# Performance work log

Measured on AMD Instinct MI355X. Metric: run time of the kernel, lower is better.

The kernel has to match this reference:

```python
import jax, jax.numpy as jnp
import numpy as np
from jax import lax

B, T, H, W, C = 32, 250, 28, 28, 1
CLASSES, IPC = 25, 10
UNITS = 512
MEM_CELLS = CLASSES * IPC  # 250
CELL = 64
HEADS = 4
FEAT = 2 * 2 * 32          # conv output flattened = 128
XDIM = FEAT + CLASSES      # 153
IN_LSTM = XDIM + HEADS * CELL  # 409
EPS_BN = 1e-3


def setup_inputs() -> dict:
    key = jax.random.key(0)
    ks = iter(jax.random.split(key, 40))
    s = 0.02
    d = {}
    d['images'] = jax.random.normal(next(ks), (B, T, H, W, C), jnp.float32)
    d['previous_labels'] = jax.random.randint(next(ks), (B, T), 0, CLASSES, jnp.int32)
    # conv stack
    for i, (ci, co) in enumerate([(1, 8), (8, 16), (16, 32)], start=1):
        d[f'k{i}'] = jax.random.normal(next(ks), (3, 3, ci, co), jnp.float32) * s
        d[f'cb{i}'] = jnp.zeros((co,), jnp.float32)
        d[f'g{i}'] = jnp.ones((co,), jnp.float32)
        d[f'be{i}'] = jnp.zeros((co,), jnp.float32)
        d[f'mm{i}'] = jnp.zeros((co,), jnp.float32)
        d[f'mv{i}'] = jnp.ones((co,), jnp.float32)
    # LSTM cell (keras gate order i,f,g,o)
    d['Wx'] = jax.random.normal(next(ks), (IN_LSTM, 4 * UNITS), jnp.float32) * s
    d['Wh'] = jax.random.normal(next(ks), (UNITS, 4 * UNITS), jnp.float32) * s
    d['bl'] = jnp.zeros((4 * UNITS,), jnp.float32)
    # parameters dense -> (read_heads+1)*cell_size, tanh
    d['Wp'] = jax.random.normal(next(ks), (UNITS, (HEADS + 1) * CELL), jnp.float32) * s
    d['bp'] = jnp.zeros(((HEADS + 1) * CELL,), jnp.float32)
    # output layer: Dense(units, tanh) on concat(h, read_value)
    d['Wo'] = jax.random.normal(next(ks), (UNITS + HEADS * CELL, UNITS), jnp.float32) * s
    d['bo'] = jnp.zeros((UNITS,), jnp.float32)
    # final classifier
    d['Wf'] = jax.random.normal(next(ks), (UNITS, CLASSES), jnp.float32) * s
    d['bf'] = jnp.zeros((CLASSES,), jnp.float32)
    return d


def _conv_bn_relu(x, k, cb, g, be, mm, mv):
    y = lax.conv_general_dilated(x, k, (2, 2), 'VALID',
                                 dimension_numbers=('NHWC', 'HWIO', 'NHWC')) + cb
    y = (y - mm) * g * lax.rsqrt(mv + EPS_BN) + be  # inference BN
    return jax.nn.relu(y)


def _l2n(x):
    return x * lax.rsqrt(jnp.maximum(jnp.sum(x * x, axis=-1, keepdims=True), 1e-12))


def _forward(images, previous_labels, k1, cb1, g1, be1, mm1, mv1,
             k2, cb2, g2, be2, mm2, mv2, k3, cb3, g3, be3, mm3, mv3,
             Wx, Wh, bl, Wp, bp, Wo, bo, Wf, bf):
    x = images.reshape(B * T, H, W, C)
    x = _conv_bn_relu(x, k1, cb1, g1, be1, mm1, mv1)
    x = _conv_bn_relu(x, k2, cb2, g2, be2, mm2, mv2)
    x = _conv_bn_relu(x, k3, cb3, g3, be3, mm3, mv3)
    x = x.reshape(B, T, FEAT)
    oh = jax.nn.one_hot(previous_labels, CLASSES, dtype=x.dtype)
    x = jnp.concatenate([x, oh], axis=-1)  # [B, T, XDIM]

    def step(carry, xt):
        h, c, rv, mem = carry
        inp = jnp.concatenate([xt, rv], axis=-1)
        z = inp @ Wx + h @ Wh + bl
        zi, zf, zg, zo = jnp.split(z, 4, axis=-1)
        i, f, g = jax.nn.sigmoid(zi), jax.nn.sigmoid(zf), jnp.tanh(zg)
        o = jax.nn.sigmoid(zo)
        c = f * c + i * g
        h = o * jnp.tanh(c)
        hid = jnp.tanh(h @ Wp + bp)
        wv = hid[:, :CELL]                                # write value
        keys = hid[:, CELL:].reshape(B, HEADS, CELL)
        att = jnp.einsum('brs,bms->brm', _l2n(keys), _l2n(mem))
        w = jax.nn.softmax(att, axis=-1)
        rv = jnp.einsum('brm,bms->brs', w, mem).reshape(B, HEADS * CELL)
        mem = jnp.concatenate([wv[:, None, :], mem[:, :-1]], axis=1)  # shift write
        out = jnp.tanh(jnp.concatenate([h, rv], axis=-1) @ Wo + bo)
        return (h, c, rv, mem), out

    carry0 = (jnp.zeros((B, UNITS)), jnp.zeros((B, UNITS)),
              jnp.zeros((B, HEADS * CELL)), jnp.zeros((B, MEM_CELLS, CELL)))
    _, ys = lax.scan(step, carry0, jnp.swapaxes(x, 0, 1))  # ys: [T, B, UNITS]
    rnn_out = jnp.swapaxes(ys, 0, 1)
    return jax.nn.softmax(rnn_out @ Wf + bf, axis=-1)


def reference(images, previous_labels, k1, cb1, g1, be1, mm1, mv1,
              k2, cb2, g2, be2, mm2, mv2, k3, cb3, g3, be3, mm3, mv3,
              Wx, Wh, bl, Wp, bp, Wo, bo, Wf, bf):
    return _forward(images, previous_labels, k1, cb1, g1, be1, mm1, mv1,
                    k2, cb2, g2, be2, mm2, mv2, k3, cb3, g3, be3, mm3, mv3,
                    Wx, Wh, bl, Wp, bp, Wo, bo, Wf, bf)
```

## Files before the change

### kernel.cpp

```cpp
#include <hip/hip_runtime.h>


constexpr size_t OFF_FEATP  = 0;
constexpr size_t OFF_WXI    = OFF_FEATP + (size_t)8000 * 128;
constexpr size_t OFF_WHI    = OFF_WXI + (size_t)409 * 2048;
constexpr size_t OFF_BLI    = OFF_WHI + (size_t)512 * 2048;
constexpr size_t OFF_ZP2A   = OFF_BLI + 2048;
constexpr size_t OFF_ZP2B   = OFF_ZP2A + 262144;
constexpr size_t OFF_OH2A   = OFF_ZP2B + 262144;
constexpr size_t OFF_OH2B   = OFF_OH2A + 65536;
constexpr size_t OFF_OUTPRE2= OFF_OH2B + 65536;
constexpr size_t OFF_HT2    = OFF_OUTPRE2 + 32768;
constexpr size_t OFF_HTT2   = OFF_HT2 + 65536;
constexpr size_t OFF_RVT2   = OFF_HTT2 + 65536;
constexpr size_t OFF_WVP2   = OFF_RVT2 + 32768;
constexpr size_t OFF_BAR    = OFF_WVP2 + 16384;
constexpr size_t OFF_WPT    = OFF_BAR + 4096;
constexpr size_t WS_FLOATS  = OFF_WPT + (size_t)163840;

constexpr int DYN_FLOATS = 34816;
constexpr int DYN_BYTES  = DYN_FLOATS * 4;

constexpr int COH = 0, COP = 512, CCO = 1024, CRING = 1536;

__device__ __forceinline__ float sigm(float x) { return 1.f / (1.f + __expf(-x)); }

typedef int iv2 __attribute__((ext_vector_type(2)));
typedef int iv4 __attribute__((ext_vector_type(4)));

__device__ __forceinline__ void st_pair(float* base, size_t pidx, float v, int tag) {
  unsigned long long u = (unsigned long long)__float_as_uint(v) |
                         ((unsigned long long)(unsigned)tag << 32);
  __hip_atomic_store((unsigned long long*)(base + 2 * pidx), u,
                     __ATOMIC_RELAXED, __HIP_MEMORY_SCOPE_AGENT);
}
__device__ __forceinline__ float spin_pair(const float* base, size_t pidx, int tag) {
  const iv2* p = (const iv2*)(base + 2 * pidx);
  iv2 v;
  for (;;) {
    asm volatile("global_load_dwordx2 %0, %1, off sc0 sc1\n\ts_waitcnt vmcnt(0)"
                 : "=&v"(v) : "v"(p) : "memory");
    if (v[1] == tag) break;
    __builtin_amdgcn_s_sleep(1);
  }
  return __int_as_float(v[0]);
}
__device__ __forceinline__ float2 spin_pair2_sum2(const float* a, const float* b, int tag) {
  const iv4* pa = (const iv4*)a;
  const iv4* pb = (const iv4*)b;
  iv4 x, y;
  for (;;) {
    asm volatile(
        "global_load_dwordx4 %0, %2, off sc0 sc1\n\t"
        "global_load_dwordx4 %1, %3, off sc0 sc1\n\t"
        "s_waitcnt vmcnt(0)"
        : "=&v"(x), "=&v"(y) : "v"(pa), "v"(pb) : "memory");
    if (x[1] == tag && x[3] == tag && y[1] == tag && y[3] == tag) break;
    __builtin_amdgcn_s_sleep(1);
  }
  return {__int_as_float(x[0]) + __int_as_float(y[0]),
          __int_as_float(x[2]) + __int_as_float(y[2])};
}
__device__ __forceinline__ float2 spin_pair_2addr(const float* a, const float* b, int tag) {
  const iv2* pa = (const iv2*)a;
  const iv2* pb = (const iv2*)b;
  iv2 x, y;
  for (;;) {
    asm volatile(
        "global_load_dwordx2 %0, %2, off sc0 sc1\n\t"
        "global_load_dwordx2 %1, %3, off sc0 sc1\n\t"
        "s_waitcnt vmcnt(0)"
        : "=&v"(x), "=&v"(y) : "v"(pa), "v"(pb) : "memory");
    if (x[1] == tag && y[1] == tag) break;
    __builtin_amdgcn_s_sleep(1);
  }
  return {__int_as_float(x[0]), __int_as_float(y[0])};
}
__device__ __forceinline__ void ld4x2_sc(const iv2* a, const iv2* b, const iv2* c,
                                         const iv2* d, iv2& x, iv2& y, iv2& z, iv2& w) {
  asm volatile(
      "global_load_dwordx2 %0, %4, off sc0 sc1\n\t"
      "global_load_dwordx2 %1, %5, off sc0 sc1\n\t"
      "global_load_dwordx2 %2, %6, off sc0 sc1\n\t"
      "global_load_dwordx2 %3, %7, off sc0 sc1\n\t"
      "s_waitcnt vmcnt(0)"
      : "=&v"(x), "=&v"(y), "=&v"(z), "=&v"(w)
      : "v"(a), "v"(b), "v"(c), "v"(d) : "memory");
}
__device__ __forceinline__ void ld8i4_sc(const iv4* b0, iv4* v) {
  const iv4 *p0 = b0, *p1 = b0 + 512, *p2 = b0 + 1024, *p3 = b0 + 1536,
            *p4 = b0 + 2048, *p5 = b0 + 2560, *p6 = b0 + 3072, *p7 = b0 + 3584;
  asm volatile(
      "global_load_dwordx4 %0, %8, off sc0 sc1\n\t"
      "global_load_dwordx4 %1, %9, off sc0 sc1\n\t"
      "global_load_dwordx4 %2, %10, off sc0 sc1\n\t"
      "global_load_dwordx4 %3, %11, off sc0 sc1\n\t"
      "global_load_dwordx4 %4, %12, off sc0 sc1\n\t"
      "global_load_dwordx4 %5, %13, off sc0 sc1\n\t"
      "global_load_dwordx4 %6, %14, off sc0 sc1\n\t"
      "global_load_dwordx4 %7, %15, off sc0 sc1\n\t"
      "s_waitcnt vmcnt(0)"
      : "=&v"(v[0]), "=&v"(v[1]), "=&v"(v[2]), "=&v"(v[3]),
        "=&v"(v[4]), "=&v"(v[5]), "=&v"(v[6]), "=&v"(v[7])
      : "v"(p0), "v"(p1), "v"(p2), "v"(p3), "v"(p4), "v"(p5), "v"(p6), "v"(p7)
      : "memory");
}
__device__ __forceinline__ void ld10i4_sc(const iv4* b0, const iv4* z0,
                                          const iv4* z1, iv4* v) {
  const iv4 *p0 = b0, *p1 = b0 + 512, *p2 = b0 + 1024, *p3 = b0 + 1536,
            *p4 = b0 + 2048, *p5 = b0 + 2560, *p6 = b0 + 3072, *p7 = b0 + 3584;
  asm volatile(
      "global_load_dwordx4 %0, %10, off sc0 sc1\n\t"
      "global_load_dwordx4 %1, %11, off sc0 sc1\n\t"
      "global_load_dwordx4 %2, %12, off sc0 sc1\n\t"
      "global_load_dwordx4 %3, %13, off sc0 sc1\n\t"
      "global_load_dwordx4 %4, %14, off sc0 sc1\n\t"
      "global_load_dwordx4 %5, %15, off sc0 sc1\n\t"
      "global_load_dwordx4 %6, %16, off sc0 sc1\n\t"
      "global_load_dwordx4 %7, %17, off sc0 sc1\n\t"
      "global_load_dwordx4 %8, %18, off sc0 sc1\n\t"
      "global_load_dwordx4 %9, %19, off sc0 sc1\n\t"
      "s_waitcnt vmcnt(0)"
      : "=&v"(v[0]), "=&v"(v[1]), "=&v"(v[2]), "=&v"(v[3]), "=&v"(v[4]),
        "=&v"(v[5]), "=&v"(v[6]), "=&v"(v[7]), "=&v"(v[8]), "=&v"(v[9])
      : "v"(p0), "v"(p1), "v"(p2), "v"(p3), "v"(p4), "v"(p5), "v"(p6), "v"(p7),
        "v"(z0), "v"(z1)
      : "memory");
}
__device__ __forceinline__ int sum8_bar(const int* b) {
  int v0, v1, v2, v3, v4, v5, v6, v7;
  asm volatile(
      "global_load_dword %0, %8, off sc0 sc1\n\t"
      "global_load_dword %1, %9, off sc0 sc1\n\t"
      "global_load_dword %2, %10, off sc0 sc1\n\t"
      "global_load_dword %3, %11, off sc0 sc1\n\t"
      "global_load_dword %4, %12, off sc0 sc1\n\t"
      "global_load_dword %5, %13, off sc0 sc1\n\t"
      "global_load_dword %6, %14, off sc0 sc1\n\t"
      "global_load_dword %7, %15, off sc0 sc1\n\t"
      "s_waitcnt vmcnt(0)"
      : "=&v"(v0), "=&v"(v1), "=&v"(v2), "=&v"(v3),
        "=&v"(v4), "=&v"(v5), "=&v"(v6), "=&v"(v7)
      : "v"(b), "v"(b + 64), "v"(b + 128), "v"(b + 192),
        "v"(b + 256), "v"(b + 320), "v"(b + 384), "v"(b + 448)
      : "memory");
  return ((v0 + v1) + (v2 + v3)) + ((v4 + v5) + (v6 + v7));
}

__global__ __launch_bounds__(256) void prep_kernel(const float* __restrict__ Wx,
                                                   const float* __restrict__ Wh,
                                                   const float* __restrict__ bl,
                                                   const float* __restrict__ Wp,
                                                   float* __restrict__ ws) {
  float* WXI = ws + OFF_WXI;
  float* WHI = ws + OFF_WHI;
  float* BLI = ws + OFF_BLI;
  float* WPT = ws + OFF_WPT;
  const int t0 = 409 * 2048;
  const int t1 = t0 + 512 * 2048;
  const int t2 = t1 + 2048;
  const int total = t2 + 163840;
  for (int idx = blockIdx.x * blockDim.x + threadIdx.x; idx < total;
       idx += gridDim.x * blockDim.x) {
    if (idx < t0) {
      int k = idx >> 11, cc = idx & 2047;
      WXI[idx] = Wx[(size_t)k * 2048 + (cc & 3) * 512 + (cc >> 2)];
    } else if (idx < t1) {
      int j = idx - t0;
      int k = j >> 11, cc = j & 2047;
      WHI[j] = Wh[(size_t)k * 2048 + (cc & 3) * 512 + (cc >> 2)];
    } else if (idx < t2) {
      int cc = idx - t1;
      BLI[cc] = bl[(cc & 3) * 512 + (cc >> 2)];
    } else {
      int e = idx - t2;
      int k4 = e / 1280, r = e - k4 * 1280;
      int j = r >> 2, ks = r & 3;
      WPT[e] = Wp[(size_t)(k4 * 4 + ks) * 320 + j];
    }
  }
}

__global__ __launch_bounds__(128) void conv_kernel(
    const float* __restrict__ img,
    const float* __restrict__ k1, const float* __restrict__ cb1, const float* __restrict__ g1,
    const float* __restrict__ be1, const float* __restrict__ mm1, const float* __restrict__ mv1,
    const float* __restrict__ k2, const float* __restrict__ cb2, const float* __restrict__ g2,
    const float* __restrict__ be2, const float* __restrict__ mm2, const float* __restrict__ mv2,
    const float* __restrict__ k3, const float* __restrict__ cb3, const float* __restrict__ g3,
    const float* __restrict__ be3, const float* __restrict__ mm3, const float* __restrict__ mv3,
    float* __restrict__ ws) {
  __shared__ float s_in[784];
  __shared__ float s_y1[13 * 13 * 8];
  __shared__ float s_y2[6 * 6 * 16];
  __shared__ float s_k1[72], s_k2[1152], s_k3[4608];
  __shared__ float s_s1[8], s_b1[8], s_s2[16], s_b2[16], s_s3[32], s_b3[32];
  float* FEATP = ws + OFF_FEATP;
  const int n = blockIdx.x, tid = threadIdx.x;
  const float* ip = img + (size_t)n * 784;
  for (int i = tid; i < 784; i += 128) s_in[i] = ip[i];
  for (int i = tid; i < 72; i += 128) s_k1[i] = k1[i];
  for (int i = tid; i < 1152; i += 128) s_k2[i] = k2[i];
  for (int i = tid; i < 4608; i += 128) s_k3[i] = k3[i];
  if (tid < 8) {
    float s = g1[tid] * rsqrtf(mv1[tid] + 1e-3f);
    s_s1[tid] = s; s_b1[tid] = (cb1[tid] - mm1[tid]) * s + be1[tid];
  } else if (tid >= 32 && tid < 48) {
    int c = tid - 32;
    float s = g2[c] * rsqrtf(mv2[c] + 1e-3f);
    s_s2[c] = s; s_b2[c] = (cb2[c] - mm2[c]) * s + be2[c];
  } else if (tid >= 64 && tid < 96) {
    int c = tid - 64;
    float s = g3[c] * rsqrtf(mv3[c] + 1e-3f);
    s_s3[c] = s; s_b3[c] = (cb3[c] - mm3[c]) * s + be3[c];
  }
  __syncthreads();
  for (int idx = tid; idx < 13 * 13 * 8; idx += 128) {
    int co = idx & 7, pos = idx >> 3;
    int j = pos % 13, i = pos / 13;
    float acc = 0.f;
    #pragma unroll
    for (int ky = 0; ky < 3; ++ky)
      #pragma unroll
      for (int kx = 0; kx < 3; ++kx)
        acc += s_in[(2 * i + ky) * 28 + (2 * j + kx)] * s_k1[(ky * 3 + kx) * 8 + co];
    float v = acc * s_s1[co] + s_b1[co];
    s_y1[idx] = v > 0.f ? v : 0.f;
  }
  __syncthreads();
  for (int idx = tid; idx < 6 * 6 * 16; idx += 128) {
    int co = idx & 15, pos = idx >> 4;
    int j = pos % 6, i = pos / 6;
    float acc = 0.f;
    for (int ky = 0; ky < 3; ++ky)
      for (int kx = 0; kx < 3; ++kx) {
        int base = ((2 * i + ky) * 13 + (2 * j + kx)) * 8;
        int kb = (ky * 3 + kx) * 128 + co;
        #pragma unroll
        for (int ci = 0; ci < 8; ++ci) acc += s_y1[base + ci] * s_k2[kb + ci * 16];
      }
    float v = acc * s_s2[co] + s_b2[co];
    s_y2[idx] = v > 0.f ? v : 0.f;
  }
  __syncthreads();
  for (int idx = tid; idx < 128; idx += 128) {
    int co = idx & 31, pos = idx >> 5;
    int j = pos & 1, i = pos >> 1;
    float acc = 0.f;
    for (int ky = 0; ky < 3; ++ky)
      for (int kx = 0; kx < 3; ++kx) {
        int base = ((2 * i + ky) * 6 + (2 * j + kx)) * 16;
        int kb = (ky * 3 + kx) * 512 + co;
        #pragma unroll
        for (int ci = 0; ci < 16; ++ci) acc += s_y2[base + ci] * s_k3[kb + ci * 32];
      }
    float v = acc * s_s3[co] + s_b3[co];
    FEATP[(size_t)n * 128 + idx] = v > 0.f ? v : 0.f;
  }
}

__global__ __launch_bounds__(512) void lstm_kernel(
    const int* __restrict__ labels,
    const float* __restrict__ Wo, const float* __restrict__ bo,
    const float* __restrict__ Wp, const float* __restrict__ bp,
    const float* __restrict__ Wf, const float* __restrict__ bf,
    float* __restrict__ ws, float* __restrict__ out) {
  extern __shared__ float dyn[];
  const float* FEATP = ws + OFF_FEATP;
  const float* WXI   = ws + OFF_WXI;
  const float* WHI   = ws + OFF_WHI;
  const float* BLI   = ws + OFF_BLI;
  float* ZP2A   = ws + OFF_ZP2A;
  float* ZP2B   = ws + OFF_ZP2B;
  float* OH2A   = ws + OFF_OH2A;
  float* OH2B   = ws + OFF_OH2B;
  float* OUTPRE2= ws + OFF_OUTPRE2;
  float* HT2    = ws + OFF_HT2;
  float* HTT2   = ws + OFF_HTT2;
  float* RVT2   = ws + OFF_RVT2;
  float* WVP2   = ws + OFF_WVP2;
  const float* WPT = ws + OFF_WPT;
  int*   BARp   = (int*)(ws + OFF_BAR);

  const int bid = blockIdx.x;
  const int tid = threadIdx.x;

  int* bc = (int*)(dyn + 34808);
  auto waitC = [&](int base, int target, int& cache) {
    if (cache >= target) return;
    if (tid == 0) {
      int v = sum8_bar(BARp + base);
      while (v < target) v = sum8_bar(BARp + base);
      bc[base >> 9] = v;
    }
    __syncthreads();
    cache = bc[base >> 9];
    __syncthreads();
  };
  auto bumpC = [&](int base) {
    asm volatile("s_waitcnt vmcnt(0)" ::: "memory");
    __syncthreads();
    if (tid == 0) atomicAdd(&BARp[base + ((bid & 7) << 6)], 1);
  };

  auto stageP = [&](float* dst, const float* srcPairs, int tag) {
    const iv4* sp = (const iv4*)srcPairs + tid;
    iv4 v[8];
    for (;;) {
      ld8i4_sc(sp, v);
      bool ok = true;
      #pragma unroll
      for (int j = 0; j < 8; ++j) ok = ok && (v[j][1] == tag) && (v[j][3] == tag);
      if (ok) break;
      __builtin_amdgcn_s_sleep(2);
    }
    #pragma unroll
    for (int j = 0; j < 8; ++j) {
      int i = (tid + j * 512) << 1;
      float2 f = {__int_as_float(v[j][0]), __int_as_float(v[j][2])};
      *(float2*)&dst[(i >> 5) * 36 + (i & 31)] = f;
    }
  };

  auto E32 = [&](const float* Wm, const float* Am, int K, float* part, float2& r) {
    const int wv = tid >> 6, l = tid & 63;
    const int ksub = l & 1, cg = (l >> 1) & 3, bg = l >> 3;
    const int Kp = K >> 4;
    const int kb = wv * (K >> 3) + ksub * Kp;
    const float* wp = Wm + (size_t)kb * 32 + cg * 8;
    const float* ap = Am + (size_t)kb * 36 + bg * 4;
    float4 acc[8];
    #pragma unroll
    for (int i = 0; i < 8; ++i) acc[i] = {0.f, 0.f, 0.f, 0.f};
    #pragma unroll 4
    for (int kk = 0; kk < Kp; ++kk) {
      float4 w0 = *(const float4*)(wp + kk * 32);
      float4 w1 = *(const float4*)(wp + kk * 32 + 4);
      float4 a  = *(const float4*)(ap + kk * 36);
      float wl[8];
      *(float4*)&wl[0] = w0; *(float4*)&wl[4] = w1;
      #pragma unroll
      for (int i = 0; i < 8; ++i) {
        acc[i].x = fmaf(wl[i], a.x, acc[i].x);
        acc[i].y = fmaf(wl[i], a.y, acc[i].y);
        acc[i].z = fmaf(wl[i], a.z, acc[i].z);
        acc[i].w = fmaf(wl[i], a.w, acc[i].w);
      }
    }
    #pragma unroll
    for (int i = 0; i < 8; ++i) {
      acc[i].x += __shfl_xor(acc[i].x, 1, 64);
      acc[i].y += __shfl_xor(acc[i].y, 1, 64);
      acc[i].z += __shfl_xor(acc[i].z, 1, 64);
      acc[i].w += __shfl_xor(acc[i].w, 1, 64);
    }
    const int ob = (cg * 8) * 36 + bg * 4;
    if (ksub == 0 && wv < 4) {
      float* pb = part + wv * 1152 + ob;
      #pragma unroll
      for (int i = 0; i < 8; ++i) *(float4*)(pb + i * 36) = acc[i];
    }
    __syncthreads();
    if (ksub == 0 && wv >= 4) {
      float* pb = part + (wv - 4) * 1152 + ob;
      #pragma unroll
      for (int i = 0; i < 8; ++i) {
        float4 t = *(float4*)(pb + i * 36);
        t.x += acc[i].x; t.y += acc[i].y; t.z += acc[i].z; t.w += acc[i].w;
        *(float4*)(pb + i * 36) = t;
      }
    }
    __syncthreads();
    const int c = tid & 31, b2 = (tid >> 5) * 2;
    const int o = c * 36 + b2;
    float2 s0 = *(float2*)(part + o);
    float2 s1 = *(float2*)(part + 1152 + o);
    float2 s2 = *(float2*)(part + 2304 + o);
    float2 s3 = *(float2*)(part + 3456 + o);
    r.x = (s0.x + s1.x) + (s2.x + s3.x);
    r.y = (s0.y + s1.y) + (s2.y + s3.y);
  };

  auto E64 = [&](const float* Wm, const float* Am, float* part, float4& r) {
    const int wv = tid >> 6, l = tid & 63;
    const int ksub = l & 1, cg = (l >> 1) & 7, bg = l >> 4;
    const int kb = wv * 32 + ksub * 16;
    const float* wp0 = Wm + (size_t)kb * 64 + ((cg * 8 + ksub * 4) & 63);
    const float* wp1 = Wm + (size_t)kb * 64 + ((cg * 8 + 4 + ksub * 4) & 63);
    const float* ap = Am + (size_t)kb * 36 + bg * 8;
    float4 acc[8][2];
    #pragma unroll
    for (int i = 0; i < 8; ++i) { acc[i][0] = {0.f,0.f,0.f,0.f}; acc[i][1] = {0.f,0.f,0.f,0.f}; }
    #pragma unroll 2
    for (int kk = 0; kk < 16; ++kk) {
      float4 w0 = *(const float4*)(wp0 + kk * 64);
      float4 w1 = *(const float4*)(wp1 + kk * 64);
      float4 a0 = *(const float4*)(ap + kk * 36);
      float4 a1 = *(const float4*)(ap + kk * 36 + 4);
      float wl[8];
      *(float4*)&wl[0] = w0; *(float4*)&wl[4] = w1;
      #pragma unroll
      for (int i = 0; i < 8; ++i) {
        acc[i][0].x = fmaf(wl[i], a0.x, acc[i][0].x);
        acc[i][0].y = fmaf(wl[i], a0.y, acc[i][0].y);
        acc[i][0].z = fmaf(wl[i], a0.z, acc[i][0].z);
        acc[i][0].w = fmaf(wl[i], a0.w, acc[i][0].w);
        acc[i][1].x = fmaf(wl[i], a1.x, acc[i][1].x);
        acc[i][1].y = fmaf(wl[i], a1.y, acc[i][1].y);
        acc[i][1].z = fmaf(wl[i], a1.z, acc[i][1].z);
        acc[i][1].w = fmaf(wl[i], a1.w, acc[i][1].w);
      }
    }
    #pragma unroll
    for (int i = 0; i < 8; ++i) {
      #pragma unroll
      for (int j = 0; j < 2; ++j) {
        acc[i][j].x += __shfl_xor(acc[i][j].x, 1, 64);
        acc[i][j].y += __shfl_xor(acc[i][j].y, 1, 64);
        acc[i][j].z += __shfl_xor(acc[i][j].z, 1, 64);
        acc[i][j].w += __shfl_xor(acc[i][j].w, 1, 64);
      }
    }
    const int ob = (cg * 8) * 36 + bg * 8;
    if (ksub == 0 && wv < 4) {
      float* pb = part + wv * 2304 + ob;
      #pragma unroll
      for (int i = 0; i < 8; ++i) {
        *(float4*)(pb + i * 36) = acc[i][0];
        *(float4*)(pb + i * 36 + 4) = acc[i][1];
      }
    }
    __syncthreads();
    if (ksub == 0 && wv >= 4) {
      float* pb = part + (wv - 4) * 2304 + ob;
      #pragma unroll
      for (int i = 0; i < 8; ++i) {
        float4 t0 = *(float4*)(pb + i * 36);
        float4 t1 = *(float4*)(pb + i * 36 + 4);
        t0.x += acc[i][0].x; t0.y += acc[i][0].y; t0.z += acc[i][0].z; t0.w += acc[i][0].w;
        t1.x += acc[i][1].x; t1.y += acc[i][1].y; t1.z += acc[i][1].z; t1.w += acc[i][1].w;
        *(float4*)(pb + i * 36) = t0;
        *(float4*)(pb + i * 36 + 4) = t1;
      }
    }
    __syncthreads();
    const int c = tid & 63, b4 = (tid >> 6) * 4;
    const int o = c * 36 + b4;
    float4 s0 = *(float4*)(part + o);
    float4 s1 = *(float4*)(part + 2304 + o);
    float4 s2 = *(float4*)(part + 4608 + o);
    float4 s3 = *(float4*)(part + 6912 + o);
    r.x = (s0.x + s1.x) + (s2.x + s3.x);
    r.y = (s0.y + s1.y) + (s2.y + s3.y);
    r.z = (s0.z + s1.z) + (s2.z + s3.z);
    r.w = (s0.w + s1.w) + (s2.w + s3.w);
  };

  if (bid < 64) {
    const int c0 = bid * 32;
    for (int i = tid; i < 8192; i += 512)
      dyn[i] = WXI[(size_t)(153 + (i >> 5)) * 2048 + c0 + (i & 31)];
    for (int i = tid; i < 4096; i += 512)
      dyn[8192 + i] = WXI[(size_t)(i >> 5) * 2048 + c0 + (i & 31)];
    if (tid < 256) dyn[12288 + tid] = 0.f;
  } else if (bid < 80) {
    const int u0 = (bid - 64) * 32;
    for (int i = tid; i < 8192; i += 512)
      dyn[i] = Wo[(size_t)(512 + (i >> 5)) * 512 + u0 + (i & 31)];
    if (tid < 32) dyn[8192 + tid] = bo[u0 + tid];
  } else if (bid < 144) {
    const int r = bid - 80;
    const int j0 = (r & 31) * 64, kh = r >> 5;
    for (int i = tid; i < 16384; i += 512) {
      int k = i >> 6, cc = i & 63;
      int cr = (cc + ((k >> 4) & 1) * 4) & 63;
      dyn[k * 64 + cr] = WHI[(size_t)(kh * 256 + k) * 2048 + j0 + cc];
    }
  } else if (bid < 160) {
    const int u0 = (bid - 144) * 32;
    for (int i = tid; i < 8192; i += 512)
      dyn[i] = Wo[(size_t)(i >> 5) * 512 + u0 + (i & 31)];
  } else if (bid < 176) {
    const int u0 = (bid - 160) * 32;
    for (int i = tid; i < 8192; i += 512)
      dyn[i] = Wo[(size_t)(256 + (i >> 5)) * 512 + u0 + (i & 31)];
  } else if (bid < 240) {
    const int hp = (bid - 176) & 1;
    for (int i = tid; i < 17000; i += 512) dyn[i] = 0.f;
    if (tid < 256) dyn[17000 + tid] = rsqrtf(1e-12f);
    if (tid < 128) dyn[21264 + tid] = bp[64 + hp * 128 + tid];
    if (tid < 64)  dyn[21392 + tid] = bp[tid];
  } else if (bid < 244) {
    const int kh = (bid - 240) >> 1, cp = (bid - 240) & 1;
    for (int i = tid; i < 8192; i += 512) {
      int k = i >> 5, c = i & 31;
      dyn[i] = Wp[(size_t)(kh * 256 + k) * 320 + cp * 32 + c];
    }
  } else if (bid < 252) {
    for (int i = tid; i < 12800; i += 512) dyn[i] = Wf[i];
    if (tid < 25) dyn[12800 + tid] = bf[tid];
  }
  __syncthreads();

  auto azPre = [&](int t) {
    const int c0 = bid * 32;
    const float* zaP = ZP2A + (t & 1) * 131072;
    const float* zbP = ZP2B + (t & 1) * 131072;
    float* zf = dyn + 27392;
    const int bb = tid >> 4, c2 = tid & 15;
    size_t pidx = (size_t)bb * 2048 + c0 + c2 * 2;
    float2 s = spin_pair2_sum2(zaP + 2 * pidx, zbP + 2 * pidx, t + 1);
    *(float2*)&zf[bb * 32 + c2 * 2] = s;
  };
  auto azGatesMain = [&](int t) {
    const float* rvP = RVT2 + ((t + 1) & 1) * 16384;
    float* Wz = dyn; float* Cst = dyn + 12288; float* rvT = dyn + 12544;
    float* zx = dyn + 26368; float* zf = dyn + 27392; float* part = dyn + 28416;
    stageP(rvT, rvP, t);
    __syncthreads();
    float2 r;
    E32(Wz, rvT, 256, part, r);
    const int c = tid & 31, b2 = (tid >> 5) * 2;
    zf[b2 * 32 + c] += r.x + zx[b2 * 32 + c];
    zf[(b2 + 1) * 32 + c] += r.y + zx[(b2 + 1) * 32 + c];
    __syncthreads();
    if (tid < 256) {
      int u = tid & 7, b = tid >> 3;
      float4 z = *(float4*)(zf + b * 32 + u * 4);
      float ig = sigm(z.x), fg = sigm(z.y), gg = tanhf(z.z), og = sigm(z.w);
      float cc = fg * Cst[b * 8 + u] + ig * gg;
      Cst[b * 8 + u] = cc;
      float hv = og * tanhf(cc);
      st_pair(HT2 + (t & 1) * 32768, (size_t)(bid * 8 + u) * 32 + b, hv, t + 1);
      st_pair(HTT2 + (t & 1) * 32768, (size_t)b * 512 + bid * 8 + u, hv, t + 1);
    }
  };
  auto azX = [&](int tt) {
    float* Wxx = dyn + 8192; float* xT = dyn + 21760;
    float* zx = dyn + 26368; float* part = dyn + 28416;
    for (int i = tid; i < 4096; i += 512) {
      int b = i >> 7, k = i & 127;
      xT[k * 36 + b] = FEATP[((size_t)b * 250 + tt) * 128 + k];
    }
    __syncthreads();
    float2 r;
    E32(Wxx, xT, 128, part, r);
    const int c = tid & 31, b2 = (tid >> 5) * 2;
    zx[b2 * 32 + c] = r.x;
    zx[(b2 + 1) * 32 + c] = r.y;
  };
  auto aoOut = [&](int t) {
    const int u0 = (bid - 64) * 32;
    const float* rvP  = RVT2 + ((t + 1) & 1) * 16384;
    const float* ohaP = OH2A + ((t + 1) & 1) * 32768;
    const float* ohbP = OH2B + ((t + 1) & 1) * 32768;
    float* W = dyn; float* bo_l = dyn + 8192; float* rvT = dyn + 8224;
    float* of = dyn + 17440; float* part = dyn + 18464;
    {
      const int b = tid >> 4, c2 = tid & 15;
      const iv4* rp = (const iv4*)rvP + tid;
      const iv4* za = (const iv4*)ohaP + (b * 256 + (u0 >> 1) + c2);
      const iv4* zb = (const iv4*)ohbP + (b * 256 + (u0 >> 1) + c2);
      iv4 v[10];
      for (;;) {
        ld10i4_sc(rp, za, zb, v);
        bool ok = true;
        #pragma unroll
        for (int j = 0; j < 10; ++j) ok = ok && (v[j][1] == t) && (v[j][3] == t);
        if (ok) break;
        __builtin_amdgcn_s_sleep(2);
      }
      #pragma unroll
      for (int j = 0; j < 8; ++j) {
        int i = (tid + j * 512) << 1;
        float2 f = {__int_as_float(v[j][0]), __int_as_float(v[j][2])};
        *(float2*)&rvT[(i >> 5) * 36 + (i & 31)] = f;
      }
      float2 s = {__int_as_float(v[8][0]) + __int_as_float(v[9][0]),
                  __int_as_float(v[8][2]) + __int_as_float(v[9][2])};
      *(float2*)&of[b * 32 + c2 * 2] = s;
    }
    __syncthreads();
    float2 r;
    E32(W, rvT, 256, part, r);
    const int c = tid & 31, b2 = (tid >> 5) * 2;
    float bv = bo_l[c];
    st_pair(OUTPRE2, (size_t)b2 * 512 + u0 + c, r.x + of[b2 * 32 + c] + bv, t);
    st_pair(OUTPRE2, (size_t)(b2 + 1) * 512 + u0 + c, r.y + of[(b2 + 1) * 32 + c] + bv, t);
  };
  auto p2Gemm = [&](int t) {
    const float* htP = HT2 + (t & 1) * 32768;
    float* W = dyn; float* A = dyn + 8192; float* part = dyn + 17408;
    const bool isOLr = bid < 160;
    stageP(A, isOLr ? htP : (htP + 16384), t + 1);
    __syncthreads();
    float2 r;
    E32(W, A, 256, part, r);
    const int c = tid & 31, b2 = (tid >> 5) * 2;
    const int u0 = (isOLr ? (bid - 144) : (bid - 160)) * 32;
    float* d = (isOLr ? OH2A : OH2B) + (t & 1) * 32768;
    st_pair(d, (size_t)b2 * 512 + u0 + c, r.x, t + 1);
    st_pair(d, (size_t)(b2 + 1) * 512 + u0 + c, r.y, t + 1);
  };

  if (bid < 64) {
    int cCOH = 0;
    azX(0);
    for (int t = 0; t < 250; ++t) {
      azPre(t);
      if (t >= 2) waitC(COH, 32 * (t - 1), cCOH);
      azGatesMain(t);
      if (t < 249) azX(t + 1);
    }
  } else if (bid < 80) {
    int cCCO = 0;
    for (int t = 1; t <= 250; ++t) {
      if (t >= 2) waitC(CCO, 8 * (t - 1), cCCO);
      aoOut(t);
      bumpC(COP);
    }
  } else if (bid < 144) {
    const int r = bid - 80;
    const int j0 = (r & 31) * 64, kh = r >> 5;
    const int c = tid & 63, b4 = (tid >> 6) * 4;
    float* W = dyn; float* A = dyn + 16384; float* part = dyn + 25600;
    float* zpBase = kh ? ZP2B : ZP2A;
    const float blv = (kh == 0) ? BLI[j0 + c] : 0.f;
    for (int s = 0; s < 250; ++s) {
      float wx0 = 0.f, wx1 = 0.f, wx2 = 0.f, wx3 = 0.f;
      if (kh == 0) {
        int l0 = labels[(b4 + 0) * 250 + s], l1 = labels[(b4 + 1) * 250 + s];
        int l2 = labels[(b4 + 2) * 250 + s], l3 = labels[(b4 + 3) * 250 + s];
        wx0 = WXI[(size_t)(128 + l0) * 2048 + j0 + c];
        wx1 = WXI[(size_t)(128 + l1) * 2048 + j0 + c];
        wx2 = WXI[(size_t)(128 + l2) * 2048 + j0 + c];
        wx3 = WXI[(size_t)(128 + l3) * 2048 + j0 + c];
      }
      stageP(A, HT2 + ((s + 1) & 1) * 32768 + kh * 16384, s);
      __syncthreads();
      float4 rr;
      E64(W, A, part, rr);
      float* zpD = zpBase + (s & 1) * 131072;
      st_pair(zpD, (size_t)(b4 + 0) * 2048 + j0 + c, rr.x + blv + wx0, s + 1);
      st_pair(zpD, (size_t)(b4 + 1) * 2048 + j0 + c, rr.y + blv + wx1, s + 1);
      st_pair(zpD, (size_t)(b4 + 2) * 2048 + j0 + c, rr.z + blv + wx2, s + 1);
      st_pair(zpD, (size_t)(b4 + 3) * 2048 + j0 + c, rr.w + blv + wx3, s + 1);
    }
  } else if (bid < 176) {
    int cCOP = 0;
    for (int t = 0; t < 250; ++t) {
      if (t >= 2) waitC(COP, 16 * (t - 1), cCOP);
      p2Gemm(t);
      bumpC(COH);
    }
  } else if (bid < 240) {
    float* ring = dyn;
    float* rn   = dyn + 17000;
    float* h_s  = dyn + 17256;
    float* kpart= dyn + 17768;
    float* kn   = dyn + 18408;
    float* att  = dyn + 18536;
    float* redS = dyn + 19068;
    float* pslab= dyn + 19088;
    float* bpk  = dyn + 21264;
    float* bpw  = dyn + 21392;
    const int b = (bid - 176) >> 1, hp = (bid - 176) & 1;
    const int j = tid & 127, q = tid >> 7;
    const int J = 64 + hp * 128 + j;
    const float4* wbase = (const float4*)WPT + q * 32 * 320 + J;
    int cCOP = 0;
    for (int t = 0; t < 250; ++t) {
      float4 pf[32];
      #pragma unroll
      for (int i = 0; i < 32; ++i) pf[i] = wbase[i * 320];
      if (t >= 2) waitC(COP, 16 * (t - 1), cCOP);
      h_s[tid] = spin_pair(HTT2 + (t & 1) * 32768, (size_t)b * 512 + tid, t + 1);
      __syncthreads();
      {
        float a = 0.f;
        #pragma unroll
        for (int i = 0; i < 32; ++i) {
          float4 h4 = *(const float4*)&h_s[q * 128 + i * 4];
          a += pf[i].x * h4.x + pf[i].y * h4.y + pf[i].z * h4.z + pf[i].w * h4.w;
        }
        kpart[q * 128 + j] = a;
      }
      __syncthreads();
      if (tid < 128) {
        float kr = kpart[tid] + kpart[128 + tid] + kpart[256 + tid] +
                   kpart[384 + tid] + bpk[tid];
        float v = tanhf(kr);
        float pq = v * v;
        #pragma unroll
        for (int off = 32; off; off >>= 1) pq += __shfl_xor(pq, off, 64);
        kn[tid] = v * rsqrtf(fmaxf(pq, 1e-12f));
      }
      __syncthreads();
      const int start = (250 - t) % 250;
      const int m = tid >> 1, hh = tid & 1;
      {
        float e = 0.f;
        if (m < 250) {
          int p = start + m; if (p >= 250) p -= 250;
          const float4* c4 = (const float4*)ring + p * 17;
          const float4* k4 = (const float4*)kn + hh * 16;
          float d = 0.f;
          #pragma unroll
          for (int s4 = 0; s4 < 16; ++s4) {
            float4 cc = c4[s4], kk = k4[s4];
            d += cc.x * kk.x + cc.y * kk.y + cc.z * kk.z + cc.w * kk.w;
          }
          e = __expf(d * rn[p]);
          att[hh * 256 + m] = e;
        }
        float sm = e;
        #pragma unroll
        for (int off = 2; off <= 32; off <<= 1) sm += __shfl_xor(sm, off, 64);
        if ((tid & 63) < 2) redS[(tid >> 6) * 2 + (tid & 1)] = sm;
      }
      __syncthreads();
      {
        int hh2 = tid >> 8, s4 = (tid >> 4) & 15, g = tid & 15;
        float4 a4 = {0.f, 0.f, 0.f, 0.f};
        for (int mm = g; mm < 250; mm += 16) {
          int p = start + mm; if (p >= 250) p -= 250;
          float w = att[hh2 * 256 + mm];
          float4 cc = ((const float4*)ring)[p * 17 + s4];
          a4.x = fmaf(w, cc.x, a4.x); a4.y = fmaf(w, cc.y, a4.y);
          a4.z = fmaf(w, cc.z, a4.z); a4.w = fmaf(w, cc.w, a4.w);
        }
        *(float4*)&pslab[(hh2 * 16 + s4) * 68 + g * 4] = a4;
      }
      __syncthreads();
      if (tid < 128) {
        int hh3 = tid >> 6, s = tid & 63;
        float denom = redS[hh3];
        #pragma unroll
        for (int w = 1; w < 8; ++w) denom += redS[w * 2 + hh3];
        float sum = 0.f;
        #pragma unroll
        for (int g = 0; g < 16; ++g)
          sum += pslab[(hh3 * 16 + (s >> 2)) * 68 + g * 4 + (s & 3)];
        st_pair(RVT2 + (t & 1) * 16384,
                (size_t)((2 * hp + hh3) * 64 + s) * 32 + b, sum / denom, t + 1);
      }
      __syncthreads();
      {
        int ip = start + 249; if (ip >= 250) ip -= 250;
        if (tid < 64) {
          float2 p01 = spin_pair_2addr(
              WVP2 + (t & 1) * 8192 + 2 * ((size_t)b * 64 + tid),
              WVP2 + (t & 1) * 8192 + 4096 + 2 * ((size_t)b * 64 + tid), t + 1);
          float nv = tanhf(p01.x + p01.y + bpw[tid]);
          ring[ip * 68 + tid] = nv;
          float n2 = nv * nv;
          #pragma unroll
          for (int off = 32; off; off >>= 1) n2 += __shfl_xor(n2, off, 64);
          if (tid == 0) rn[ip] = rsqrtf(fmaxf(n2, 1e-12f));
        }
      }
      bumpC(CRING);
    }
  } else if (bid < 244) {
    const int kh = (bid - 240) >> 1, cp = (bid - 240) & 1;
    float* W = dyn; float* A = dyn + 8192; float* part = dyn + 17408;
    int cCR = 0;
    for (int t = 0; t < 250; ++t) {
      if (t >= 2) waitC(CRING, 64 * (t - 1), cCR);
      stageP(A, HT2 + (t & 1) * 32768 + kh * 16384, t + 1);
      __syncthreads();
      float2 r;
      E32(W, A, 256, part, r);
      const int c = tid & 31, b2 = (tid >> 5) * 2;
      float* d = WVP2 + (t & 1) * 8192 + kh * 4096;
      st_pair(d, (size_t)b2 * 64 + cp * 32 + c, r.x, t + 1);
      st_pair(d, (size_t)(b2 + 1) * 64 + cp * 32 + c, r.y, t + 1);
    }
  } else if (bid < 252) {
    const int b0 = (bid - 244) * 4;
    float* WfL = dyn; float* bfL = dyn + 12800;
    float* to4 = dyn + 12832;
    float* lp  = dyn + 14880;
    float* lg  = dyn + 15280;
    for (int t = 1; t <= 250; ++t) {
      {
        const iv2* p0 = (const iv2*)(OUTPRE2 + 2 * ((size_t)(b0 + 0) * 512 + tid));
        const iv2* p1 = (const iv2*)(OUTPRE2 + 2 * ((size_t)(b0 + 1) * 512 + tid));
        const iv2* p2 = (const iv2*)(OUTPRE2 + 2 * ((size_t)(b0 + 2) * 512 + tid));
        const iv2* p3 = (const iv2*)(OUTPRE2 + 2 * ((size_t)(b0 + 3) * 512 + tid));
        iv2 v0, v1, v2, v3;
        for (;;) {
          ld4x2_sc(p0, p1, p2, p3, v0, v1, v2, v3);
          if (v0[1] == t && v1[1] == t && v2[1] == t && v3[1] == t) break;
          __builtin_amdgcn_s_sleep(2);
        }
        to4[tid]        = tanhf(__int_as_float(v0[0]));
        to4[512 + tid]  = tanhf(__int_as_float(v1[0]));
        to4[1024 + tid] = tanhf(__int_as_float(v2[0]));
        to4[1536 + tid] = tanhf(__int_as_float(v3[0]));
      }
      __syncthreads();
      for (int i = 0; i < 4; ++i) {
        float* to = to4 + i * 512;
        if (tid < 400) {
          int l = tid % 25, p = tid / 25;
          float s = 0.f;
          #pragma unroll
          for (int q = 0; q < 32; ++q) { int k = p * 32 + q; s += to[k] * WfL[k * 25 + l]; }
          lp[p * 25 + l] = s;
        }
        __syncthreads();
        if (tid < 25) {
          float s = bfL[tid];
          #pragma unroll
          for (int p = 0; p < 16; ++p) s += lp[p * 25 + tid];
          lg[tid] = s;
        }
        __syncthreads();
        if (tid == 0) {
          float mx = lg[0];
          for (int l = 1; l < 25; ++l) mx = fmaxf(mx, lg[l]);
          float ss = 0.f;
          for (int l = 0; l < 25; ++l) ss += __expf(lg[l] - mx);
          lg[25] = mx; lg[26] = 1.f / ss;
        }
        __syncthreads();
        if (tid < 25)
          out[((size_t)(b0 + i) * 250 + (t - 1)) * 25 + tid] =
              __expf(lg[tid] - lg[25]) * lg[26];
        __syncthreads();
      }
      bumpC(CCO);
    }
  }
}

extern "C" void kernel_launch(void* const* d_in, const int* in_sizes, int n_in,
                              void* d_out, int out_size, void* d_ws, size_t ws_size,
                              hipStream_t stream) {
  const float* images = (const float*)d_in[0];
  const int* labels = (const int*)d_in[1];
  const float* k1  = (const float*)d_in[2];
  const float* cb1 = (const float*)d_in[3];
  const float* g1  = (const float*)d_in[4];
  const float* be1 = (const float*)d_in[5];
  const float* mm1 = (const float*)d_in[6];
  const float* mv1 = (const float*)d_in[7];
  const float* k2  = (const float*)d_in[8];
  const float* cb2 = (const float*)d_in[9];
  const float* g2  = (const float*)d_in[10];
  const float* be2 = (const float*)d_in[11];
  const float* mm2 = (const float*)d_in[12];
  const float* mv2 = (const float*)d_in[13];
  const float* k3  = (const float*)d_in[14];
  const float* cb3 = (const float*)d_in[15];
  const float* g3  = (const float*)d_in[16];
  const float* be3 = (const float*)d_in[17];
  const float* mm3 = (const float*)d_in[18];
  const float* mv3 = (const float*)d_in[19];
  const float* Wx  = (const float*)d_in[20];
  const float* Wh  = (const float*)d_in[21];
  const float* bl  = (const float*)d_in[22];
  const float* Wp  = (const float*)d_in[23];
  const float* bp  = (const float*)d_in[24];
  const float* Wo  = (const float*)d_in[25];
  const float* bo  = (const float*)d_in[26];
  const float* Wf  = (const float*)d_in[27];
  const float* bf  = (const float*)d_in[28];
  float* ws = (float*)d_ws;

  hipFuncSetAttribute((const void*)lstm_kernel,
                      hipFuncAttributeMaxDynamicSharedMemorySize, DYN_BYTES);

  hipMemsetAsync((char*)d_ws + OFF_ZP2A * sizeof(float), 0,
                 (OFF_WPT - OFF_ZP2A) * sizeof(float), stream);
  prep_kernel<<<1024, 256, 0, stream>>>(Wx, Wh, bl, Wp, ws);
  conv_kernel<<<8000, 128, 0, stream>>>(images,
      k1, cb1, g1, be1, mm1, mv1,
      k2, cb2, g2, be2, mm2, mv2,
      k3, cb3, g3, be3, mm3, mv3, ws);
  lstm_kernel<<<256, 512, DYN_BYTES, stream>>>(labels, Wo, bo, Wp, bp, Wf, bf, ws,
                                               (float*)d_out);
}
```

Measured before the change: 3.844 ms.

## Skip zero memory slots in attention, merge rv/z polling, trim key prefetch

In the read-attention blocks, memory slots that have not been written yet (indices at or above t) are known to be zero. Their dot products and weighted sums are skipped, and each contributes exp(0)=1 straight to the softmax denominator, which also removes the modular ring indexing. The LSTM gate blocks now poll the read-vector and both z-partial buffers in one combined spin loop with a single batched load, instead of staging them separately. The key-projection loop prefetches only half of its weight float4s into registers and streams the rest, which lowers register pressure but adds loads inside the critical step.

Result: no change. 3.825 ms (-0.5%).

```diff
diff --git a/kernel.cpp b/kernel.cpp
--- a/kernel.cpp
+++ b/kernel.cpp
@@ -27,6 +27,7 @@
 
 typedef int iv2 __attribute__((ext_vector_type(2)));
 typedef int iv4 __attribute__((ext_vector_type(4)));
+typedef float fv4 __attribute__((ext_vector_type(4)));
 
 __device__ __forceinline__ void st_pair(float* base, size_t pidx, float v, int tag) {
   unsigned long long u = (unsigned long long)__float_as_uint(v) |
@@ -44,22 +45,6 @@
     __builtin_amdgcn_s_sleep(1);
   }
   return __int_as_float(v[0]);
-}
-__device__ __forceinline__ float2 spin_pair2_sum2(const float* a, const float* b, int tag) {
-  const iv4* pa = (const iv4*)a;
-  const iv4* pb = (const iv4*)b;
-  iv4 x, y;
-  for (;;) {
-    asm volatile(
-        "global_load_dwordx4 %0, %2, off sc0 sc1\n\t"
-        "global_load_dwordx4 %1, %3, off sc0 sc1\n\t"
-        "s_waitcnt vmcnt(0)"
-        : "=&v"(x), "=&v"(y) : "v"(pa), "v"(pb) : "memory");
-    if (x[1] == tag && x[3] == tag && y[1] == tag && y[3] == tag) break;
-    __builtin_amdgcn_s_sleep(1);
-  }
-  return {__int_as_float(x[0]) + __int_as_float(y[0]),
-          __int_as_float(x[2]) + __int_as_float(y[2])};
 }
 __device__ __forceinline__ float2 spin_pair_2addr(const float* a, const float* b, int tag) {
   const iv2* pa = (const iv2*)a;
@@ -502,38 +487,36 @@
   }
   __syncthreads();
 
-  auto azPre = [&](int t) {
-    const int c0 = bid * 32;
+  auto azStage = [&](int t) {
+    const float* rvP = RVT2 + ((t + 1) & 1) * 16384;
     const float* zaP = ZP2A + (t & 1) * 131072;
     const float* zbP = ZP2B + (t & 1) * 131072;
-    float* zf = dyn + 27392;
+    float* rvT = dyn + 12544; float* zf = dyn + 27392;
     const int bb = tid >> 4, c2 = tid & 15;
-    size_t pidx = (size_t)bb * 2048 + c0 + c2 * 2;
-    float2 s = spin_pair2_sum2(zaP + 2 * pidx, zbP + 2 * pidx, t + 1);
+    const iv4* rp = (const iv4*)rvP + tid;
+    const size_t zi = (size_t)bb * 1024 + bid * 16 + c2;
+    const iv4* za = (const iv4*)zaP + zi;
+    const iv4* zb = (const iv4*)zbP + zi;
+    iv4 v[10];
+    for (;;) {
+      ld10i4_sc(rp, za, zb, v);
+      bool ok = true;
+      #pragma unroll
+      for (int j = 0; j < 8; ++j) ok = ok && (v[j][1] == t) && (v[j][3] == t);
+      ok = ok && (v[8][1] == t + 1) && (v[8][3] == t + 1) &&
+                 (v[9][1] == t + 1) && (v[9][3] == t + 1);
+      if (ok) break;
+      __builtin_amdgcn_s_sleep(1);
+    }
+    #pragma unroll
+    for (int j = 0; j < 8; ++j) {
+      int i = (tid + j * 512) << 1;
+      float2 f = {__int_as_float(v[j][0]), __int_as_float(v[j][2])};
+      *(float2*)&rvT[(i >> 5) * 36 + (i & 31)] = f;
+    }
+    float2 s = {__int_as_float(v[8][0]) + __int_as_float(v[9][0]),
+                __int_as_float(v[8][2]) + __int_as_float(v[9][2])};
     *(float2*)&zf[bb * 32 + c2 * 2] = s;
-  };
-  auto azGatesMain = [&](int t) {
-    const float* rvP = RVT2 + ((t + 1) & 1) * 16384;
-    float* Wz = dyn; float* Cst = dyn + 12288; float* rvT = dyn + 12544;
-    float* zx = dyn + 26368; float* zf = dyn + 27392; float* part = dyn + 28416;
-    stageP(rvT, rvP, t);
-    __syncthreads();
-    float2 r;
-    E32(Wz, rvT, 256, part, r);
-    const int c = tid & 31, b2 = (tid >> 5) * 2;
-    zf[b2 * 32 + c] += r.x + zx[b2 * 32 + c];
-    zf[(b2 + 1) * 32 + c] += r.y + zx[(b2 + 1) * 32 + c];
-    __syncthreads();
-    if (tid < 256) {
-      int u = tid & 7, b = tid >> 3;
-      float4 z = *(float4*)(zf + b * 32 + u * 4);
-      float ig = sigm(z.x), fg = sigm(z.y), gg = tanhf(z.z), og = sigm(z.w);
-      float cc = fg * Cst[b * 8 + u] + ig * gg;
-      Cst[b * 8 + u] = cc;
-      float hv = og * tanhf(cc);
-      st_pair(HT2 + (t & 1) * 32768, (size_t)(bid * 8 + u) * 32 + b, hv, t + 1);
-      st_pair(HTT2 + (t & 1) * 32768, (size_t)b * 512 + bid * 8 + u, hv, t + 1);
-    }
   };
   auto azX = [&](int tt) {
     float* Wxx = dyn + 8192; float* xT = dyn + 21760;
@@ -605,11 +588,29 @@
 
   if (bid < 64) {
     int cCOH = 0;
+    float* Wz = dyn; float* Cst = dyn + 12288; float* rvT = dyn + 12544;
+    float* zx = dyn + 26368; float* zf = dyn + 27392; float* part = dyn + 28416;
     azX(0);
     for (int t = 0; t < 250; ++t) {
-      azPre(t);
+      azStage(t);
       if (t >= 2) waitC(COH, 32 * (t - 1), cCOH);
-      azGatesMain(t);
+      __syncthreads();
+      float2 r;
+      E32(Wz, rvT, 256, part, r);
+      const int c = tid & 31, b2 = (tid >> 5) * 2;
+      zf[b2 * 32 + c] += r.x + zx[b2 * 32 + c];
+      zf[(b2 + 1) * 32 + c] += r.y + zx[(b2 + 1) * 32 + c];
+      __syncthreads();
+      if (tid < 256) {
+        int u = tid & 7, b = tid >> 3;
+        float4 z = *(float4*)(zf + b * 32 + u * 4);
+        float ig = sigm(z.x), fg = sigm(z.y), gg = tanhf(z.z), og = sigm(z.w);
+        float cc = fg * Cst[b * 8 + u] + ig * gg;
+        Cst[b * 8 + u] = cc;
+        float hv = og * tanhf(cc);
+        st_pair(HT2 + (t & 1) * 32768, (size_t)(bid * 8 + u) * 32 + b, hv, t + 1);
+        st_pair(HTT2 + (t & 1) * 32768, (size_t)b * 512 + bid * 8 + u, hv, t + 1);
+      }
       if (t < 249) azX(t + 1);
     }
   } else if (bid < 80) {
@@ -667,21 +668,31 @@
     const int b = (bid - 176) >> 1, hp = (bid - 176) & 1;
     const int j = tid & 127, q = tid >> 7;
     const int J = 64 + hp * 128 + j;
-    const float4* wbase = (const float4*)WPT + q * 32 * 320 + J;
+    const fv4* wbase = (const fv4*)WPT + q * 32 * 320 + J;
     int cCOP = 0;
     for (int t = 0; t < 250; ++t) {
-      float4 pf[32];
-      #pragma unroll
-      for (int i = 0; i < 32; ++i) pf[i] = wbase[i * 320];
+      fv4 pf[16];
+      #pragma unroll
+      for (int i = 0; i < 16; ++i) pf[i] = wbase[i * 320];
+      asm volatile("" :: "v"(pf[0]), "v"(pf[1]), "v"(pf[2]), "v"(pf[3]),
+                         "v"(pf[4]), "v"(pf[5]), "v"(pf[6]), "v"(pf[7]),
+                         "v"(pf[8]), "v"(pf[9]), "v"(pf[10]), "v"(pf[11]),
+                         "v"(pf[12]), "v"(pf[13]), "v"(pf[14]), "v"(pf[15]));
       if (t >= 2) waitC(COP, 16 * (t - 1), cCOP);
       h_s[tid] = spin_pair(HTT2 + (t & 1) * 32768, (size_t)b * 512 + tid, t + 1);
       __syncthreads();
       {
         float a = 0.f;
         #pragma unroll
-        for (int i = 0; i < 32; ++i) {
-          float4 h4 = *(const float4*)&h_s[q * 128 + i * 4];
+        for (int i = 0; i < 16; ++i) {
+          fv4 h4 = *(const fv4*)&h_s[q * 128 + i * 4];
           a += pf[i].x * h4.x + pf[i].y * h4.y + pf[i].z * h4.z + pf[i].w * h4.w;
+        }
+        #pragma unroll 4
+        for (int i = 16; i < 32; ++i) {
+          fv4 w4 = wbase[i * 320];
+          fv4 h4 = *(const fv4*)&h_s[q * 128 + i * 4];
+          a += w4.x * h4.x + w4.y * h4.y + w4.z * h4.z + w4.w * h4.w;
         }
         kpart[q * 128 + j] = a;
       }
@@ -696,13 +707,12 @@
         kn[tid] = v * rsqrtf(fmaxf(pq, 1e-12f));
       }
       __syncthreads();
-      const int start = (250 - t) % 250;
+      const int start = 250 - t;
       const int m = tid >> 1, hh = tid & 1;
       {
         float e = 0.f;
-        if (m < 250) {
-          int p = start + m; if (p >= 250) p -= 250;
-          const float4* c4 = (const float4*)ring + p * 17;
+        if (m < t) {
+          const float4* c4 = (const float4*)ring + (start + m) * 17;
           const float4* k4 = (const float4*)kn + hh * 16;
           float d = 0.f;
           #pragma unroll
@@ -710,8 +720,10 @@
             float4 cc = c4[s4], kk = k4[s4];
             d += cc.x * kk.x + cc.y * kk.y + cc.z * kk.z + cc.w * kk.w;
           }
-          e = __expf(d * rn[p]);
+          e = __expf(d * rn[start + m]);
           att[hh * 256 + m] = e;
+        } else if (m < 250) {
+          e = 1.f;
         }
         float sm = e;
         #pragma unroll
@@ -722,10 +734,9 @@
       {
         int hh2 = tid >> 8, s4 = (tid >> 4) & 15, g = tid & 15;
         float4 a4 = {0.f, 0.f, 0.f, 0.f};
-        for (int mm = g; mm < 250; mm += 16) {
-          int p = start + mm; if (p >= 250) p -= 250;
+        for (int mm = g; mm < t; mm += 16) {
           float w = att[hh2 * 256 + mm];
-          float4 cc = ((const float4*)ring)[p * 17 + s4];
+          float4 cc = ((const float4*)ring)[(start + mm) * 17 + s4];
           a4.x = fmaf(w, cc.x, a4.x); a4.y = fmaf(w, cc.y, a4.y);
           a4.z = fmaf(w, cc.z, a4.z); a4.w = fmaf(w, cc.w, a4.w);
         }
@@ -746,7 +757,7 @@
       }
       __syncthreads();
       {
-        int ip = start + 249; if (ip >= 250) ip -= 250;
+        const int ip = 249 - t;
         if (tid < 64) {
           float2 p01 = spin_pair_2addr(
               WVP2 + (t & 1) * 8192 + 2 * ((size_t)b * 64 + tid),
```
